# Kernel optimization log

Hardware: AMD Instinct MI355X
Metric: run time of the kernel (lower is better)

Reference implementation:

```python
import jax, jax.numpy as jnp
import numpy as np

NEG_SLOPE = 0.2


def gat_conv(x, src, dst, W, a_src, a_dst, bias, n_nodes):
    # PyG GATConv (heads=1): h = xW; e_ij = LeakyReLU(a_src.h_j + a_dst.h_i)
    # softmax over incoming edges per destination node, then scatter-sum.
    h = x @ W                                  # [N, F]
    alpha_s = h @ a_src                        # [N]
    alpha_d = h @ a_dst                        # [N]
    e = jax.nn.leaky_relu(alpha_s[src] + alpha_d[dst], NEG_SLOPE)  # [E]
    m = jax.ops.segment_max(e, dst, num_segments=n_nodes)
    ex = jnp.exp(e - m[dst])
    denom = jax.ops.segment_sum(ex, dst, num_segments=n_nodes)
    alpha = ex / denom[dst]                    # [E]
    out = jax.ops.segment_sum(alpha[:, None] * h[src], dst, num_segments=n_nodes)
    return out + bias


def setup_inputs() -> dict:
    key = jax.random.key(0)
    ks = jax.random.split(key, 16)
    N, E, F_in = 50000, 800000, 256
    x = jax.random.normal(ks[0], (N, F_in), dtype=jnp.float32)
    edge_index = jax.random.randint(ks[1], (2, E), 0, N, dtype=jnp.int64)

    def glorot(k, shape):
        fan_in, fan_out = shape[0], shape[-1]
        s = jnp.sqrt(6.0 / (fan_in + fan_out))
        return jax.random.uniform(k, shape, jnp.float32, -s, s)

    params = dict(
        W1=glorot(ks[2], (F_in, 128)),
        a1s=glorot(ks[3], (128,)),
        a1d=glorot(ks[4], (128,)),
        b1=jnp.zeros((128,), jnp.float32),
        Wl=glorot(ks[5], (128, 32)),
        bl=jnp.zeros((32,), jnp.float32),
        W2=glorot(ks[6], (32, 16)),
        a2s=glorot(ks[7], (16,)),
        a2d=glorot(ks[8], (16,)),
        b2=jnp.zeros((16,), jnp.float32),
        Wm=glorot(ks[9], (16, 1)),
        bm=jnp.zeros((1,), jnp.float32),
    )
    return {"x": x, "edge_index": edge_index, **params}


def reference(x, edge_index, W1, a1s, a1d, b1, Wl, bl, W2, a2s, a2d, b2, Wm, bm):
    n = x.shape[0]
    loops = jnp.arange(n, dtype=edge_index.dtype)
    src = jnp.concatenate([edge_index[0], loops])  # add_self_loops=True
    dst = jnp.concatenate([edge_index[1], loops])

    h = jax.nn.relu(gat_conv(x, src, dst, W1, a1s, a1d, b1, n))
    h = h @ Wl + bl
    h = jax.nn.relu(gat_conv(h, src, dst, W2, a2s, a2d, b2, n))
    out = h @ Wm + bm                             # MLP([16,1]) = single Linear
    return out.squeeze()
```

## Files before the change

kernel.cpp:

```cpp
#include <hip/hip_runtime.h>
#include <math.h>


#define NEG_SLOPE 0.2f

#define BSHIFT 8
#define BCAP   6144
#define BCAPC  (BCAP + 256)

typedef __attribute__((ext_vector_type(8))) short bf16x8;
typedef __attribute__((ext_vector_type(4))) float f32x4;
typedef __attribute__((ext_vector_type(8))) _Float16 h16x8;

__device__ __forceinline__ unsigned short bf_hi(float f) {
    unsigned u = __float_as_uint(f);
    return (unsigned short)((u + 0x7fffu + ((u >> 16) & 1u)) >> 16);
}
__device__ __forceinline__ float bf_tof(unsigned short s) {
    return __uint_as_float(((unsigned)s) << 16);
}
__device__ __forceinline__ float leaky(float e) {
    return e > 0.f ? e : NEG_SLOPE * e;
}


__launch_bounds__(256)
__global__ void k_bin(const int* __restrict__ src_e, const int* __restrict__ dst_e,
                      int E, int* __restrict__ gcur, unsigned* __restrict__ binned) {
    __shared__ int scnt[256];
    __shared__ int sbase[256];
    int tid = threadIdx.x;
    scnt[tid] = 0;
    __syncthreads();
    int base_e = blockIdx.x * 4096;
    int myd[16];
#pragma unroll
    for (int k = 0; k < 16; ++k) {
        int j = base_e + k * 256 + tid;
        if (j < E) {
            int d = dst_e[j];
            myd[k] = d;
            atomicAdd(&scnt[d >> BSHIFT], 1);
        } else myd[k] = -1;
    }
    __syncthreads();
    int c = scnt[tid];
    sbase[tid] = c ? atomicAdd(&gcur[tid], c) : 0;
    scnt[tid] = 0;
    __syncthreads();
#pragma unroll
    for (int k = 0; k < 16; ++k) {
        int j = base_e + k * 256 + tid;
        if (j >= E) continue;
        int d = myd[k];
        int b = d >> BSHIFT;
        int off = sbase[b] + atomicAdd(&scnt[b], 1);
        if (off < BCAP)
            binned[(size_t)b * BCAP + off] = ((unsigned)src_e[j] << BSHIFT) | (unsigned)(d & 255);
    }
}

__launch_bounds__(256)
__global__ void k_csr(const unsigned* __restrict__ binned, const int* __restrict__ gcur,
                      int N, int* __restrict__ csr, int* __restrict__ rowptr,
                      int* __restrict__ rowend) {
    __shared__ int sdeg[256], s[256], scur[256];
    int b = blockIdx.x, tid = threadIdx.x;
    int node0 = b << BSHIFT;
    int nloc = N - node0; if (nloc > 256) nloc = 256;
    int cnt = gcur[b]; if (cnt > BCAP) cnt = BCAP;
    sdeg[tid] = (tid < nloc) ? 1 : 0;
    __syncthreads();
    const unsigned* bp = binned + (size_t)b * BCAP;
    for (int j = tid; j < cnt; j += 256) atomicAdd(&sdeg[bp[j] & 255], 1);
    __syncthreads();
    int v = sdeg[tid];
    s[tid] = v;
    __syncthreads();
    for (int off = 1; off < 256; off <<= 1) {
        int t = (tid >= off) ? s[tid - off] : 0;
        __syncthreads();
        s[tid] += t;
        __syncthreads();
    }
    int excl = s[tid] - v;
    int rowbase = b * BCAPC;
    if (tid < nloc) {
        rowptr[node0 + tid] = rowbase + excl;
        rowend[node0 + tid] = rowbase + excl + v;
        csr[rowbase + excl] = node0 + tid;
    }
    scur[tid] = excl + 1;
    __syncthreads();
    for (int j = tid; j < cnt; j += 256) {
        unsigned p = bp[j];
        int pos = atomicAdd(&scur[p & 255], 1);
        csr[rowbase + pos] = (int)(p >> BSHIFT);
    }
}


__global__ void k_wcvt(const float* __restrict__ W, short* __restrict__ Wt_hi,
                       short* __restrict__ Wt_lo, int* __restrict__ gcur) {
    if (blockIdx.x == 0) gcur[threadIdx.x] = 0;
    int i = blockIdx.x * 256 + threadIdx.x;
    int k = i >> 7, c = i & 127;
    float v = W[i];
    unsigned short h = bf_hi(v);
    unsigned short l = bf_hi(v - bf_tof(h));
    Wt_hi[c * 256 + k] = (short)h;
    Wt_lo[c * 256 + k] = (short)l;
}


#define LDST 40

__launch_bounds__(256)
__global__ void k_gemm1_mfma(const float* __restrict__ x, const short* __restrict__ Wt_hi,
                             const short* __restrict__ Wt_lo,
                             const float* __restrict__ a1s, const float* __restrict__ a1d,
                             int N, _Float16* __restrict__ h1h,
                             float* __restrict__ as1, float* __restrict__ ad1) {
    __shared__ short Ah[64 * LDST], Al[64 * LDST];
    __shared__ short Bh[128 * LDST], Bl[128 * LDST];
    int tid = threadIdx.x;
    int w = tid >> 6, lane = tid & 63;
    int rowbase = blockIdx.x * 64;

    f32x4 acc[8];
#pragma unroll
    for (int c = 0; c < 8; ++c) acc[c] = (f32x4){0.f, 0.f, 0.f, 0.f};

    int arow = tid >> 2;
    int aq   = tid & 3;
    int agrow = rowbase + arow;
    int fr = lane & 15;
    int fk = lane >> 4;

    for (int ks = 0; ks < 8; ++ks) {
        int k0 = ks * 32;
        __syncthreads();
        {
            float4 u0 = make_float4(0.f, 0.f, 0.f, 0.f), u1 = u0;
            if (agrow < N) {
                const float* p = x + (size_t)agrow * 256 + k0 + aq * 8;
                u0 = *(const float4*)p;
                u1 = *(const float4*)(p + 4);
            }
            float f[8] = {u0.x, u0.y, u0.z, u0.w, u1.x, u1.y, u1.z, u1.w};
            bf16x8 hv, lv;
#pragma unroll
            for (int j = 0; j < 8; ++j) {
                unsigned short h = bf_hi(f[j]);
                unsigned short l = bf_hi(f[j] - bf_tof(h));
                hv[j] = (short)h;
                lv[j] = (short)l;
            }
            *(bf16x8*)&Ah[arow * LDST + aq * 8] = hv;
            *(bf16x8*)&Al[arow * LDST + aq * 8] = lv;
        }
        {
#pragma unroll
            for (int rep = 0; rep < 2; ++rep) {
                int ci = tid + rep * 256;
                int row = ci >> 2, q = ci & 3;
                const short* ph = Wt_hi + row * 256 + k0 + q * 8;
                const short* pl = Wt_lo + row * 256 + k0 + q * 8;
                *(bf16x8*)&Bh[row * LDST + q * 8] = *(const bf16x8*)ph;
                *(bf16x8*)&Bl[row * LDST + q * 8] = *(const bf16x8*)pl;
            }
        }
        __syncthreads();
        bf16x8 a_h = *(const bf16x8*)&Ah[(w * 16 + fr) * LDST + fk * 8];
        bf16x8 a_l = *(const bf16x8*)&Al[(w * 16 + fr) * LDST + fk * 8];
#pragma unroll
        for (int c = 0; c < 8; ++c) {
            bf16x8 b_h = *(const bf16x8*)&Bh[(c * 16 + fr) * LDST + fk * 8];
            bf16x8 b_l = *(const bf16x8*)&Bl[(c * 16 + fr) * LDST + fk * 8];
            acc[c] = __builtin_amdgcn_mfma_f32_16x16x32_bf16(a_h, b_h, acc[c], 0, 0, 0);
            acc[c] = __builtin_amdgcn_mfma_f32_16x16x32_bf16(a_l, b_h, acc[c], 0, 0, 0);
            acc[c] = __builtin_amdgcn_mfma_f32_16x16x32_bf16(a_h, b_l, acc[c], 0, 0, 0);
        }
    }

    float s_[4] = {0.f, 0.f, 0.f, 0.f};
    float d_[4] = {0.f, 0.f, 0.f, 0.f};
#pragma unroll
    for (int c = 0; c < 8; ++c) {
        int col = c * 16 + fr;
        float av = a1s[col], dv = a1d[col];
#pragma unroll
        for (int r = 0; r < 4; ++r) {
            s_[r] += acc[c][r] * av;
            d_[r] += acc[c][r] * dv;
        }
    }
#pragma unroll
    for (int off = 1; off < 16; off <<= 1) {
#pragma unroll
        for (int r = 0; r < 4; ++r) {
            s_[r] += __shfl_xor(s_[r], off);
            d_[r] += __shfl_xor(d_[r], off);
        }
    }
#pragma unroll
    for (int r = 0; r < 4; ++r) {
        int grow = rowbase + w * 16 + fk * 4 + r;
        if (grow < N) {
            _Float16* dst = h1h + (size_t)grow * 128;
#pragma unroll
            for (int c = 0; c < 8; ++c) dst[c * 16 + fr] = (_Float16)acc[c][r];
        }
    }
    if (fr == 0) {
#pragma unroll
        for (int r = 0; r < 4; ++r) {
            int grow = rowbase + w * 16 + fk * 4 + r;
            if (grow < N) { as1[grow] = s_[r]; ad1[grow] = d_[r]; }
        }
    }
}


__global__ void k_agg1(const _Float16* __restrict__ h1h, const float* __restrict__ as1,
                       const float* __restrict__ ad1, const int* __restrict__ rowptr,
                       const int* __restrict__ rowend,
                       const int* __restrict__ csr, const float* __restrict__ b1,
                       int N, float* __restrict__ out1) {
    int wid = (blockIdx.x * blockDim.x + threadIdx.x) >> 6;
    int lane = threadIdx.x & 63;
    if (wid >= N) return;
    int beg = rowptr[wid], end = rowend[wid];
    int cnt = end - beg;
    float adn = ad1[wid];

    int smine = 0;
    float wmine = 0.f;
    if (lane < cnt) {
        smine = csr[beg + lane];
        wmine = __expf(leaky(as1[smine] + adn));
    }
    float den = wmine;
    for (int idx = lane + 64; idx < cnt; idx += 64)
        den += __expf(leaky(as1[csr[beg + idx]] + adn));
#pragma unroll
    for (int off = 32; off; off >>= 1) den += __shfl_xor(den, off);
    float inv = 1.f / den;

    int g = lane >> 4;
    int f8 = lane & 15;
    float acc[8];
#pragma unroll
    for (int k = 0; k < 8; ++k) acc[k] = 0.f;

    int lim = cnt < 64 ? cnt : 64;
    int jb = 0;
    for (; jb + 12 < lim; jb += 16) {
        int j = jb + g;
        int s0 = __shfl(smine, j);
        int s1 = __shfl(smine, j + 4);
        int s2 = __shfl(smine, j + 8);
        int s3 = __shfl(smine, j + 12);
        float w0 = __shfl(wmine, j);
        float w1 = __shfl(wmine, j + 4);
        float w2 = __shfl(wmine, j + 8);
        float w3 = __shfl(wmine, j + 12);
        h16x8 v0 = *(const h16x8*)(h1h + (size_t)s0 * 128 + f8 * 8);
        h16x8 v1 = *(const h16x8*)(h1h + (size_t)s1 * 128 + f8 * 8);
        h16x8 v2 = *(const h16x8*)(h1h + (size_t)s2 * 128 + f8 * 8);
        h16x8 v3 = *(const h16x8*)(h1h + (size_t)s3 * 128 + f8 * 8);
#pragma unroll
        for (int k = 0; k < 8; ++k)
            acc[k] += w0 * (float)v0[k] + w1 * (float)v1[k]
                    + w2 * (float)v2[k] + w3 * (float)v3[k];
    }
    for (; jb < lim; jb += 4) {
        int j = jb + g;
        int s0 = __shfl(smine, j);
        float w0 = __shfl(wmine, j);
        h16x8 v0 = *(const h16x8*)(h1h + (size_t)s0 * 128 + f8 * 8);
#pragma unroll
        for (int k = 0; k < 8; ++k) acc[k] += w0 * (float)v0[k];
    }
    for (int j = 64 + g; j < cnt; j += 4) {
        int s0 = csr[beg + j];
        float w0 = __expf(leaky(as1[s0] + adn));
        h16x8 v0 = *(const h16x8*)(h1h + (size_t)s0 * 128 + f8 * 8);
#pragma unroll
        for (int k = 0; k < 8; ++k) acc[k] += w0 * (float)v0[k];
    }
#pragma unroll
    for (int off = 16; off <= 32; off <<= 1) {
#pragma unroll
        for (int k = 0; k < 8; ++k) acc[k] += __shfl_xor(acc[k], off);
    }
    if (g == 0) {
        const float* bb = b1 + f8 * 8;
        float o[8];
#pragma unroll
        for (int k = 0; k < 8; ++k) o[k] = fmaxf(acc[k] * inv + bb[k], 0.f);
        float* dst = out1 + (size_t)wid * 128 + f8 * 8;
        *(float4*)dst = make_float4(o[0], o[1], o[2], o[3]);
        *(float4*)(dst + 4) = make_float4(o[4], o[5], o[6], o[7]);
    }
}


__launch_bounds__(256)
__global__ void k_mlp(const float* __restrict__ out1, const float* __restrict__ Wl,
                      const float* __restrict__ bl, const float* __restrict__ W2,
                      const float* __restrict__ a2s, const float* __restrict__ a2d,
                      int N, float* __restrict__ h3,
                      float* __restrict__ as2, float* __restrict__ ad2) {
    __shared__ float sWl[128 * 32];
    __shared__ float sW2[32 * 16];
    __shared__ float sbl[32];
    __shared__ float sa2s[16];
    __shared__ float sa2d[16];
    int tid = threadIdx.x;
    for (int i = tid; i < 128 * 32; i += blockDim.x) sWl[i] = Wl[i];
    for (int i = tid; i < 32 * 16; i += blockDim.x) sW2[i] = W2[i];
    if (tid < 32) sbl[tid] = bl[tid];
    if (tid < 16) { sa2s[tid] = a2s[tid]; sa2d[tid] = a2d[tid]; }
    __syncthreads();
    int n = blockIdx.x * blockDim.x + tid;
    if (n >= N) return;

    float h2[32];
#pragma unroll
    for (int j = 0; j < 32; ++j) h2[j] = sbl[j];
    const float4* row = (const float4*)(out1 + (size_t)n * 128);
    for (int k4 = 0; k4 < 32; ++k4) {
        float4 v = row[k4];
        const float* w0 = &sWl[(k4 * 4 + 0) * 32];
        const float* w1 = &sWl[(k4 * 4 + 1) * 32];
        const float* w2 = &sWl[(k4 * 4 + 2) * 32];
        const float* w3 = &sWl[(k4 * 4 + 3) * 32];
#pragma unroll
        for (int j = 0; j < 32; ++j)
            h2[j] += v.x * w0[j] + v.y * w1[j] + v.z * w2[j] + v.w * w3[j];
    }
    float h3l[16];
#pragma unroll
    for (int j = 0; j < 16; ++j) h3l[j] = 0.f;
#pragma unroll
    for (int k = 0; k < 32; ++k) {
        float hv = h2[k];
#pragma unroll
        for (int j = 0; j < 16; ++j) h3l[j] += hv * sW2[k * 16 + j];
    }
    float s = 0.f, d = 0.f;
#pragma unroll
    for (int j = 0; j < 16; ++j) { s += h3l[j] * sa2s[j]; d += h3l[j] * sa2d[j]; }
    float4* h3row = (float4*)(h3 + (size_t)n * 16);
    h3row[0] = make_float4(h3l[0], h3l[1], h3l[2], h3l[3]);
    h3row[1] = make_float4(h3l[4], h3l[5], h3l[6], h3l[7]);
    h3row[2] = make_float4(h3l[8], h3l[9], h3l[10], h3l[11]);
    h3row[3] = make_float4(h3l[12], h3l[13], h3l[14], h3l[15]);
    as2[n] = s;
    ad2[n] = d;
}


__global__ void k_agg2(const float* __restrict__ h3, const float* __restrict__ as2,
                       const float* __restrict__ ad2, const int* __restrict__ rowptr,
                       const int* __restrict__ rowend,
                       const int* __restrict__ csr, const float* __restrict__ b2,
                       const float* __restrict__ Wm, const float* __restrict__ bm,
                       int N, float* __restrict__ out) {
    int wid = (blockIdx.x * blockDim.x + threadIdx.x) >> 6;
    int lane = threadIdx.x & 63;
    if (wid >= N) return;
    int beg = rowptr[wid], end = rowend[wid];
    int cnt = end - beg;
    float adn = ad2[wid];

    int smine = 0;
    float wmine = 0.f;
    if (lane < cnt) {
        smine = csr[beg + lane];
        wmine = __expf(leaky(as2[smine] + adn));
    }
    float den = wmine;
    for (int idx = lane + 64; idx < cnt; idx += 64)
        den += __expf(leaky(as2[csr[beg + idx]] + adn));
#pragma unroll
    for (int off = 32; off; off >>= 1) den += __shfl_xor(den, off);
    float inv = 1.f / den;

    int eg = lane >> 2;
    int f4 = lane & 3;
    float4 acc = make_float4(0.f, 0.f, 0.f, 0.f);
    int lim = cnt < 64 ? cnt : 64;
    int jb = 0;
    for (; jb + 16 < lim; jb += 32) {
        int j = jb + eg;
        int s0 = __shfl(smine, j);
        int s1 = __shfl(smine, j + 16);
        float w0 = __shfl(wmine, j);
        float w1 = __shfl(wmine, j + 16);
        float4 v0 = ((const float4*)(h3 + (size_t)s0 * 16))[f4];
        float4 v1 = ((const float4*)(h3 + (size_t)s1 * 16))[f4];
        acc.x += w0 * v0.x + w1 * v1.x;
        acc.y += w0 * v0.y + w1 * v1.y;
        acc.z += w0 * v0.z + w1 * v1.z;
        acc.w += w0 * v0.w + w1 * v1.w;
    }
    for (; jb < lim; jb += 16) {
        int j = jb + eg;
        int s0 = __shfl(smine, j);
        float w0 = __shfl(wmine, j);
        float4 v0 = ((const float4*)(h3 + (size_t)s0 * 16))[f4];
        acc.x += w0 * v0.x; acc.y += w0 * v0.y;
        acc.z += w0 * v0.z; acc.w += w0 * v0.w;
    }
    for (int j = 64 + eg; j < cnt; j += 16) {
        int s0 = csr[beg + j];
        float w0 = __expf(leaky(as2[s0] + adn));
        float4 v0 = ((const float4*)(h3 + (size_t)s0 * 16))[f4];
        acc.x += w0 * v0.x; acc.y += w0 * v0.y;
        acc.z += w0 * v0.z; acc.w += w0 * v0.w;
    }
#pragma unroll
    for (int off = 4; off <= 32; off <<= 1) {
        acc.x += __shfl_xor(acc.x, off);
        acc.y += __shfl_xor(acc.y, off);
        acc.z += __shfl_xor(acc.z, off);
        acc.w += __shfl_xor(acc.w, off);
    }
    float4 bb = ((const float4*)b2)[f4];
    float4 wm = ((const float4*)Wm)[f4];
    float o0 = fmaxf(acc.x * inv + bb.x, 0.f);
    float o1 = fmaxf(acc.y * inv + bb.y, 0.f);
    float o2 = fmaxf(acc.z * inv + bb.z, 0.f);
    float o3 = fmaxf(acc.w * inv + bb.w, 0.f);
    float v = o0 * wm.x + o1 * wm.y + o2 * wm.z + o3 * wm.w;
    v += __shfl_xor(v, 1);
    v += __shfl_xor(v, 2);
    if (lane == 0) out[wid] = v + bm[0];
}


extern "C" void kernel_launch(void* const* d_in, const int* in_sizes, int n_in,
                              void* d_out, int out_size, void* d_ws, size_t ws_size,
                              hipStream_t stream) {
    const float* x   = (const float*)d_in[0];
    const int*   ei  = (const int*)d_in[1];
    const float* W1  = (const float*)d_in[2];
    const float* a1s = (const float*)d_in[3];
    const float* a1d = (const float*)d_in[4];
    const float* b1  = (const float*)d_in[5];
    const float* Wl  = (const float*)d_in[6];
    const float* bl  = (const float*)d_in[7];
    const float* W2  = (const float*)d_in[8];
    const float* a2s = (const float*)d_in[9];
    const float* a2d = (const float*)d_in[10];
    const float* b2  = (const float*)d_in[11];
    const float* Wm  = (const float*)d_in[12];
    const float* bm  = (const float*)d_in[13];

    int N  = in_sizes[0] / 256;
    int E  = in_sizes[1] / 2;
    int nbuck = (N + 255) >> BSHIFT;
    float* out = (float*)d_out;

    char* w = (char*)d_ws;
    auto alloc = [&](size_t bytes) -> char* {
        char* p = w;
        w += (bytes + 255) & ~(size_t)255;
        return p;
    };
    _Float16* h1h = (_Float16*)alloc((size_t)N * 128 * 2);
    float* out1   = (float*)alloc((size_t)N * 128 * 4);
    float* h3     = (float*)alloc((size_t)N * 16 * 4);
    float* as1    = (float*)alloc((size_t)N * 4);
    float* ad1    = (float*)alloc((size_t)N * 4);
    float* as2    = (float*)alloc((size_t)N * 4);
    float* ad2    = (float*)alloc((size_t)N * 4);
    int*   rowptr = (int*)alloc((size_t)N * 4);
    int*   rowend = (int*)alloc((size_t)N * 4);
    int*   gcur   = (int*)alloc(256 * 4);
    short* Wt_hi  = (short*)alloc((size_t)128 * 256 * 2);
    short* Wt_lo  = (short*)alloc((size_t)128 * 256 * 2);
    unsigned* binned = (unsigned*)alloc((size_t)nbuck * BCAP * 4);
    int*   csr    = (int*)alloc((size_t)nbuck * BCAPC * 4);

    const int* src_e = ei;
    const int* dst_e = ei + E;

    k_wcvt<<<128, 256, 0, stream>>>(W1, Wt_hi, Wt_lo, gcur);
    k_bin<<<(E + 4095) / 4096, 256, 0, stream>>>(src_e, dst_e, E, gcur, binned);
    k_csr<<<nbuck, 256, 0, stream>>>(binned, gcur, N, csr, rowptr, rowend);

    k_gemm1_mfma<<<(N + 63) / 64, 256, 0, stream>>>(x, Wt_hi, Wt_lo, a1s, a1d,
                                                    N, h1h, as1, ad1);
    k_agg1<<<(N + 3) / 4, 256, 0, stream>>>(h1h, as1, ad1, rowptr, rowend, csr, b1, N, out1);
    k_mlp<<<(N + 255) / 256, 256, 0, stream>>>(out1, Wl, bl, W2, a2s, a2d, N, h3, as2, ad2);
    k_agg2<<<(N + 3) / 4, 256, 0, stream>>>(h3, as2, ad2, rowptr, rowend, csr, b2, Wm, bm, N, out);
}
```

Measured before the change: 144.3 us.

## Fuse MLP layer into first aggregation kernel and shrink binning blocks

The linear layer, second GAT projection and attention-score computation are folded into the layer-1 aggregation kernel, so the 128-wide fp32 intermediate no longer goes to global memory and the separate MLP launch is gone. Each wave computes its node's 128->32->16 projection cooperatively using shuffle reductions, with the weights staged in shared memory. Every agg1 block now loads about 18KB of weights into LDS (50000/4 blocks), which adds load traffic and may reduce occupancy. Separately, the binning kernel handles 1024 edges per block instead of 4096, giving more blocks to spread across the GPU.

```diff
diff --git a/kernel.cpp b/kernel.cpp
--- a/kernel.cpp
+++ b/kernel.cpp
@@ -32,10 +32,10 @@
     int tid = threadIdx.x;
     scnt[tid] = 0;
     __syncthreads();
-    int base_e = blockIdx.x * 4096;
-    int myd[16];
-#pragma unroll
-    for (int k = 0; k < 16; ++k) {
+    int base_e = blockIdx.x * 1024;
+    int myd[4];
+#pragma unroll
+    for (int k = 0; k < 4; ++k) {
         int j = base_e + k * 256 + tid;
         if (j < E) {
             int d = dst_e[j];
@@ -49,7 +49,7 @@
     scnt[tid] = 0;
     __syncthreads();
 #pragma unroll
-    for (int k = 0; k < 16; ++k) {
+    for (int k = 0; k < 4; ++k) {
         int j = base_e + k * 256 + tid;
         if (j >= E) continue;
         int d = myd[k];
@@ -222,13 +222,30 @@
 }
 
 
+__launch_bounds__(256)
 __global__ void k_agg1(const _Float16* __restrict__ h1h, const float* __restrict__ as1,
                        const float* __restrict__ ad1, const int* __restrict__ rowptr,
-                       const int* __restrict__ rowend,
-                       const int* __restrict__ csr, const float* __restrict__ b1,
-                       int N, float* __restrict__ out1) {
-    int wid = (blockIdx.x * blockDim.x + threadIdx.x) >> 6;
-    int lane = threadIdx.x & 63;
+                       const int* __restrict__ rowend, const int* __restrict__ csr,
+                       const float* __restrict__ b1, const float* __restrict__ Wl,
+                       const float* __restrict__ bl, const float* __restrict__ W2,
+                       const float* __restrict__ a2s, const float* __restrict__ a2d,
+                       int N, float* __restrict__ h3,
+                       float* __restrict__ as2, float* __restrict__ ad2) {
+    __shared__ float sWl[128 * 32];
+    __shared__ float sW2[32 * 16];
+    __shared__ float sb1[128];
+    __shared__ float sbl[32];
+    __shared__ float sa2s[16], sa2d[16];
+    int tid = threadIdx.x;
+    for (int i = tid; i < 128 * 32; i += 256) sWl[i] = Wl[i];
+    for (int i = tid; i < 32 * 16; i += 256) sW2[i] = W2[i];
+    if (tid < 128) sb1[tid] = b1[tid];
+    if (tid < 32) sbl[tid] = bl[tid];
+    if (tid < 16) { sa2s[tid] = a2s[tid]; sa2d[tid] = a2d[tid]; }
+    __syncthreads();
+
+    int wid = (blockIdx.x * blockDim.x + tid) >> 6;
+    int lane = tid & 63;
     if (wid >= N) return;
     int beg = rowptr[wid], end = rowend[wid];
     int cnt = end - beg;
@@ -294,71 +311,66 @@
 #pragma unroll
         for (int k = 0; k < 8; ++k) acc[k] += __shfl_xor(acc[k], off);
     }
-    if (g == 0) {
-        const float* bb = b1 + f8 * 8;
-        float o[8];
-#pragma unroll
-        for (int k = 0; k < 8; ++k) o[k] = fmaxf(acc[k] * inv + bb[k], 0.f);
-        float* dst = out1 + (size_t)wid * 128 + f8 * 8;
-        *(float4*)dst = make_float4(o[0], o[1], o[2], o[3]);
-        *(float4*)(dst + 4) = make_float4(o[4], o[5], o[6], o[7]);
-    }
-}
-
-
-__launch_bounds__(256)
-__global__ void k_mlp(const float* __restrict__ out1, const float* __restrict__ Wl,
-                      const float* __restrict__ bl, const float* __restrict__ W2,
-                      const float* __restrict__ a2s, const float* __restrict__ a2d,
-                      int N, float* __restrict__ h3,
-                      float* __restrict__ as2, float* __restrict__ ad2) {
-    __shared__ float sWl[128 * 32];
-    __shared__ float sW2[32 * 16];
-    __shared__ float sbl[32];
-    __shared__ float sa2s[16];
-    __shared__ float sa2d[16];
-    int tid = threadIdx.x;
-    for (int i = tid; i < 128 * 32; i += blockDim.x) sWl[i] = Wl[i];
-    for (int i = tid; i < 32 * 16; i += blockDim.x) sW2[i] = W2[i];
-    if (tid < 32) sbl[tid] = bl[tid];
-    if (tid < 16) { sa2s[tid] = a2s[tid]; sa2d[tid] = a2d[tid]; }
-    __syncthreads();
-    int n = blockIdx.x * blockDim.x + tid;
-    if (n >= N) return;
-
-    float h2[32];
-#pragma unroll
-    for (int j = 0; j < 32; ++j) h2[j] = sbl[j];
-    const float4* row = (const float4*)(out1 + (size_t)n * 128);
-    for (int k4 = 0; k4 < 32; ++k4) {
-        float4 v = row[k4];
-        const float* w0 = &sWl[(k4 * 4 + 0) * 32];
-        const float* w1 = &sWl[(k4 * 4 + 1) * 32];
-        const float* w2 = &sWl[(k4 * 4 + 2) * 32];
-        const float* w3 = &sWl[(k4 * 4 + 3) * 32];
-#pragma unroll
-        for (int j = 0; j < 32; ++j)
-            h2[j] += v.x * w0[j] + v.y * w1[j] + v.z * w2[j] + v.w * w3[j];
-    }
+
+    float o[8];
+#pragma unroll
+    for (int k = 0; k < 8; ++k) o[k] = fmaxf(acc[k] * inv + sb1[f8 * 8 + k], 0.f);
+
+    float h2[8];
+#pragma unroll
+    for (int j = 0; j < 8; ++j) h2[j] = 0.f;
+#pragma unroll
+    for (int k = 0; k < 8; ++k) {
+        float ov = o[k];
+        const float* wr = &sWl[(f8 * 8 + k) * 32 + g * 8];
+        float4 wa = *(const float4*)wr;
+        float4 wb = *(const float4*)(wr + 4);
+        h2[0] += ov * wa.x; h2[1] += ov * wa.y; h2[2] += ov * wa.z; h2[3] += ov * wa.w;
+        h2[4] += ov * wb.x; h2[5] += ov * wb.y; h2[6] += ov * wb.z; h2[7] += ov * wb.w;
+    }
+#pragma unroll
+    for (int off = 1; off <= 8; off <<= 1) {
+#pragma unroll
+        for (int j = 0; j < 8; ++j) h2[j] += __shfl_xor(h2[j], off);
+    }
+#pragma unroll
+    for (int j = 0; j < 8; ++j) h2[j] += sbl[g * 8 + j];
+
     float h3l[16];
 #pragma unroll
     for (int j = 0; j < 16; ++j) h3l[j] = 0.f;
 #pragma unroll
-    for (int k = 0; k < 32; ++k) {
+    for (int k = 0; k < 8; ++k) {
         float hv = h2[k];
-#pragma unroll
-        for (int j = 0; j < 16; ++j) h3l[j] += hv * sW2[k * 16 + j];
-    }
+        const float* wr = &sW2[(g * 8 + k) * 16];
+        float4 wa = *(const float4*)wr;
+        float4 wb = *(const float4*)(wr + 4);
+        float4 wc = *(const float4*)(wr + 8);
+        float4 wd = *(const float4*)(wr + 12);
+        h3l[0]  += hv * wa.x; h3l[1]  += hv * wa.y; h3l[2]  += hv * wa.z; h3l[3]  += hv * wa.w;
+        h3l[4]  += hv * wb.x; h3l[5]  += hv * wb.y; h3l[6]  += hv * wb.z; h3l[7]  += hv * wb.w;
+        h3l[8]  += hv * wc.x; h3l[9]  += hv * wc.y; h3l[10] += hv * wc.z; h3l[11] += hv * wc.w;
+        h3l[12] += hv * wd.x; h3l[13] += hv * wd.y; h3l[14] += hv * wd.z; h3l[15] += hv * wd.w;
+    }
+#pragma unroll
+    for (int off = 16; off <= 32; off <<= 1) {
+#pragma unroll
+        for (int j = 0; j < 16; ++j) h3l[j] += __shfl_xor(h3l[j], off);
+    }
+
     float s = 0.f, d = 0.f;
 #pragma unroll
     for (int j = 0; j < 16; ++j) { s += h3l[j] * sa2s[j]; d += h3l[j] * sa2d[j]; }
-    float4* h3row = (float4*)(h3 + (size_t)n * 16);
-    h3row[0] = make_float4(h3l[0], h3l[1], h3l[2], h3l[3]);
-    h3row[1] = make_float4(h3l[4], h3l[5], h3l[6], h3l[7]);
-    h3row[2] = make_float4(h3l[8], h3l[9], h3l[10], h3l[11]);
-    h3row[3] = make_float4(h3l[12], h3l[13], h3l[14], h3l[15]);
-    as2[n] = s;
-    ad2[n] = d;
+
+    if (lane == 0) {
+        float* hp = h3 + (size_t)wid * 16;
+        *(float4*)(hp + 0)  = make_float4(h3l[0], h3l[1], h3l[2], h3l[3]);
+        *(float4*)(hp + 4)  = make_float4(h3l[4], h3l[5], h3l[6], h3l[7]);
+        *(float4*)(hp + 8)  = make_float4(h3l[8], h3l[9], h3l[10], h3l[11]);
+        *(float4*)(hp + 12) = make_float4(h3l[12], h3l[13], h3l[14], h3l[15]);
+        as2[wid] = s;
+        ad2[wid] = d;
+    }
 }
 
 
@@ -471,7 +483,6 @@
         return p;
     };
     _Float16* h1h = (_Float16*)alloc((size_t)N * 128 * 2);
-    float* out1   = (float*)alloc((size_t)N * 128 * 4);
     float* h3     = (float*)alloc((size_t)N * 16 * 4);
     float* as1    = (float*)alloc((size_t)N * 4);
     float* ad1    = (float*)alloc((size_t)N * 4);
@@ -489,12 +500,14 @@
     const int* dst_e = ei + E;
 
     k_wcvt<<<128, 256, 0, stream>>>(W1, Wt_hi, Wt_lo, gcur);
-    k_bin<<<(E + 4095) / 4096, 256, 0, stream>>>(src_e, dst_e, E, gcur, binned);
+    k_bin<<<(E + 1023) / 1024, 256, 0, stream>>>(src_e, dst_e, E, gcur, binned);
     k_csr<<<nbuck, 256, 0, stream>>>(binned, gcur, N, csr, rowptr, rowend);
 
     k_gemm1_mfma<<<(N + 63) / 64, 256, 0, stream>>>(x, Wt_hi, Wt_lo, a1s, a1d,
                                                     N, h1h, as1, ad1);
-    k_agg1<<<(N + 3) / 4, 256, 0, stream>>>(h1h, as1, ad1, rowptr, rowend, csr, b1, N, out1);
-    k_mlp<<<(N + 255) / 256, 256, 0, stream>>>(out1, Wl, bl, W2, a2s, a2d, N, h3, as2, ad2);
-    k_agg2<<<(N + 3) / 4, 256, 0, stream>>>(h3, as2, ad2, rowptr, rowend, csr, b2, Wm, bm, N, out);
-}
+    k_agg1<<<(N + 3) / 4, 256, 0, stream>>>(h1h, as1, ad1, rowptr, rowend, csr,
+                                            b1, Wl, bl, W2, a2s, a2d,
+                                            N, h3, as2, ad2);
+    k_agg2<<<(N + 3) / 4, 256, 0, stream>>>(h3, as2, ad2, rowptr, rowend, csr,
+                                            b2, Wm, bm, N, out);
+}
```

Measured after the change: 216.0 us. +49.7%, slower.

## Merge CSR build and first GEMM into one launch, defer denominator reduction

Applied to the files above, without the earlier changes.

The CSR construction and the first-layer MFMA GEMM are independent, so they now run as one kernel. The first nbuck blocks build the CSR and the remaining blocks do the GEMM, with shared memory overlaid through a union. This removes one launch and its serialization gap, and lets the small CSR grid (196 blocks) overlap with the GEMM blocks. Separately, the softmax denominator's cross-lane shuffle reduction in both aggregation kernels is moved after the feature accumulation, which may let it overlap with the gather latency. The cost is a larger shared-memory footprint for CSR blocks and branch divergence at block level.

```diff
diff --git a/kernel.cpp b/kernel.cpp
--- a/kernel.cpp
+++ b/kernel.cpp
@@ -60,45 +60,6 @@
     }
 }
 
-__launch_bounds__(256)
-__global__ void k_csr(const unsigned* __restrict__ binned, const int* __restrict__ gcur,
-                      int N, int* __restrict__ csr, int* __restrict__ rowptr,
-                      int* __restrict__ rowend) {
-    __shared__ int sdeg[256], s[256], scur[256];
-    int b = blockIdx.x, tid = threadIdx.x;
-    int node0 = b << BSHIFT;
-    int nloc = N - node0; if (nloc > 256) nloc = 256;
-    int cnt = gcur[b]; if (cnt > BCAP) cnt = BCAP;
-    sdeg[tid] = (tid < nloc) ? 1 : 0;
-    __syncthreads();
-    const unsigned* bp = binned + (size_t)b * BCAP;
-    for (int j = tid; j < cnt; j += 256) atomicAdd(&sdeg[bp[j] & 255], 1);
-    __syncthreads();
-    int v = sdeg[tid];
-    s[tid] = v;
-    __syncthreads();
-    for (int off = 1; off < 256; off <<= 1) {
-        int t = (tid >= off) ? s[tid - off] : 0;
-        __syncthreads();
-        s[tid] += t;
-        __syncthreads();
-    }
-    int excl = s[tid] - v;
-    int rowbase = b * BCAPC;
-    if (tid < nloc) {
-        rowptr[node0 + tid] = rowbase + excl;
-        rowend[node0 + tid] = rowbase + excl + v;
-        csr[rowbase + excl] = node0 + tid;
-    }
-    scur[tid] = excl + 1;
-    __syncthreads();
-    for (int j = tid; j < cnt; j += 256) {
-        unsigned p = bp[j];
-        int pos = atomicAdd(&scur[p & 255], 1);
-        csr[rowbase + pos] = (int)(p >> BSHIFT);
-    }
-}
-
 
 __global__ void k_wcvt(const float* __restrict__ W, short* __restrict__ Wt_hi,
                        short* __restrict__ Wt_lo, int* __restrict__ gcur) {
@@ -116,16 +77,58 @@
 #define LDST 40
 
 __launch_bounds__(256)
-__global__ void k_gemm1_mfma(const float* __restrict__ x, const short* __restrict__ Wt_hi,
-                             const short* __restrict__ Wt_lo,
-                             const float* __restrict__ a1s, const float* __restrict__ a1d,
-                             int N, _Float16* __restrict__ h1h,
-                             float* __restrict__ as1, float* __restrict__ ad1) {
-    __shared__ short Ah[64 * LDST], Al[64 * LDST];
-    __shared__ short Bh[128 * LDST], Bl[128 * LDST];
+__global__ void k_csr_gemm(const unsigned* __restrict__ binned, const int* __restrict__ gcur,
+                           int* __restrict__ csr, int* __restrict__ rowptr,
+                           int* __restrict__ rowend, int nbuck,
+                           const float* __restrict__ x, const short* __restrict__ Wt_hi,
+                           const short* __restrict__ Wt_lo,
+                           const float* __restrict__ a1s, const float* __restrict__ a1d,
+                           int N, _Float16* __restrict__ h1h,
+                           float* __restrict__ as1, float* __restrict__ ad1) {
+    __shared__ union {
+        struct { int sdeg[256], s[256], scur[256]; } c;
+        struct { short Ah[64 * LDST], Al[64 * LDST], Bh[128 * LDST], Bl[128 * LDST]; } g;
+    } sm;
     int tid = threadIdx.x;
+
+    if (blockIdx.x < (unsigned)nbuck) {
+        int b = blockIdx.x;
+        int node0 = b << BSHIFT;
+        int nloc = N - node0; if (nloc > 256) nloc = 256;
+        int cnt = gcur[b]; if (cnt > BCAP) cnt = BCAP;
+        sm.c.sdeg[tid] = (tid < nloc) ? 1 : 0;
+        __syncthreads();
+        const unsigned* bp = binned + (size_t)b * BCAP;
+        for (int j = tid; j < cnt; j += 256) atomicAdd(&sm.c.sdeg[bp[j] & 255], 1);
+        __syncthreads();
+        int v = sm.c.sdeg[tid];
+        sm.c.s[tid] = v;
+        __syncthreads();
+        for (int off = 1; off < 256; off <<= 1) {
+            int t = (tid >= off) ? sm.c.s[tid - off] : 0;
+            __syncthreads();
+            sm.c.s[tid] += t;
+            __syncthreads();
+        }
+        int excl = sm.c.s[tid] - v;
+        int rowbase = b * BCAPC;
+        if (tid < nloc) {
+            rowptr[node0 + tid] = rowbase + excl;
+            rowend[node0 + tid] = rowbase + excl + v;
+            csr[rowbase + excl] = node0 + tid;
+        }
+        sm.c.scur[tid] = excl + 1;
+        __syncthreads();
+        for (int j = tid; j < cnt; j += 256) {
+            unsigned p = bp[j];
+            int pos = atomicAdd(&sm.c.scur[p & 255], 1);
+            csr[rowbase + pos] = (int)(p >> BSHIFT);
+        }
+        return;
+    }
+
     int w = tid >> 6, lane = tid & 63;
-    int rowbase = blockIdx.x * 64;
+    int rowbase = (blockIdx.x - nbuck) * 64;
 
     f32x4 acc[8];
 #pragma unroll
@@ -156,8 +159,8 @@
                 hv[j] = (short)h;
                 lv[j] = (short)l;
             }
-            *(bf16x8*)&Ah[arow * LDST + aq * 8] = hv;
-            *(bf16x8*)&Al[arow * LDST + aq * 8] = lv;
+            *(bf16x8*)&sm.g.Ah[arow * LDST + aq * 8] = hv;
+            *(bf16x8*)&sm.g.Al[arow * LDST + aq * 8] = lv;
         }
         {
 #pragma unroll
@@ -166,17 +169,17 @@
                 int row = ci >> 2, q = ci & 3;
                 const short* ph = Wt_hi + row * 256 + k0 + q * 8;
                 const short* pl = Wt_lo + row * 256 + k0 + q * 8;
-                *(bf16x8*)&Bh[row * LDST + q * 8] = *(const bf16x8*)ph;
-                *(bf16x8*)&Bl[row * LDST + q * 8] = *(const bf16x8*)pl;
+                *(bf16x8*)&sm.g.Bh[row * LDST + q * 8] = *(const bf16x8*)ph;
+                *(bf16x8*)&sm.g.Bl[row * LDST + q * 8] = *(const bf16x8*)pl;
             }
         }
         __syncthreads();
-        bf16x8 a_h = *(const bf16x8*)&Ah[(w * 16 + fr) * LDST + fk * 8];
-        bf16x8 a_l = *(const bf16x8*)&Al[(w * 16 + fr) * LDST + fk * 8];
+        bf16x8 a_h = *(const bf16x8*)&sm.g.Ah[(w * 16 + fr) * LDST + fk * 8];
+        bf16x8 a_l = *(const bf16x8*)&sm.g.Al[(w * 16 + fr) * LDST + fk * 8];
 #pragma unroll
         for (int c = 0; c < 8; ++c) {
-            bf16x8 b_h = *(const bf16x8*)&Bh[(c * 16 + fr) * LDST + fk * 8];
-            bf16x8 b_l = *(const bf16x8*)&Bl[(c * 16 + fr) * LDST + fk * 8];
+            bf16x8 b_h = *(const bf16x8*)&sm.g.Bh[(c * 16 + fr) * LDST + fk * 8];
+            bf16x8 b_l = *(const bf16x8*)&sm.g.Bl[(c * 16 + fr) * LDST + fk * 8];
             acc[c] = __builtin_amdgcn_mfma_f32_16x16x32_bf16(a_h, b_h, acc[c], 0, 0, 0);
             acc[c] = __builtin_amdgcn_mfma_f32_16x16x32_bf16(a_l, b_h, acc[c], 0, 0, 0);
             acc[c] = __builtin_amdgcn_mfma_f32_16x16x32_bf16(a_h, b_l, acc[c], 0, 0, 0);
@@ -243,9 +246,6 @@
     float den = wmine;
     for (int idx = lane + 64; idx < cnt; idx += 64)
         den += __expf(leaky(as1[csr[beg + idx]] + adn));
-#pragma unroll
-    for (int off = 32; off; off >>= 1) den += __shfl_xor(den, off);
-    float inv = 1.f / den;
 
     int g = lane >> 4;
     int f8 = lane & 15;
@@ -294,6 +294,10 @@
 #pragma unroll
         for (int k = 0; k < 8; ++k) acc[k] += __shfl_xor(acc[k], off);
     }
+#pragma unroll
+    for (int off = 32; off; off >>= 1) den += __shfl_xor(den, off);
+    float inv = 1.f / den;
+
     if (g == 0) {
         const float* bb = b1 + f8 * 8;
         float o[8];
@@ -384,9 +388,6 @@
     float den = wmine;
     for (int idx = lane + 64; idx < cnt; idx += 64)
         den += __expf(leaky(as2[csr[beg + idx]] + adn));
-#pragma unroll
-    for (int off = 32; off; off >>= 1) den += __shfl_xor(den, off);
-    float inv = 1.f / den;
 
     int eg = lane >> 2;
     int f4 = lane & 3;
@@ -428,6 +429,10 @@
         acc.z += __shfl_xor(acc.z, off);
         acc.w += __shfl_xor(acc.w, off);
     }
+#pragma unroll
+    for (int off = 32; off; off >>= 1) den += __shfl_xor(den, off);
+    float inv = 1.f / den;
+
     float4 bb = ((const float4*)b2)[f4];
     float4 wm = ((const float4*)Wm)[f4];
     float o0 = fmaxf(acc.x * inv + bb.x, 0.f);
@@ -490,10 +495,12 @@
 
     k_wcvt<<<128, 256, 0, stream>>>(W1, Wt_hi, Wt_lo, gcur);
     k_bin<<<(E + 4095) / 4096, 256, 0, stream>>>(src_e, dst_e, E, gcur, binned);
-    k_csr<<<nbuck, 256, 0, stream>>>(binned, gcur, N, csr, rowptr, rowend);
-
-    k_gemm1_mfma<<<(N + 63) / 64, 256, 0, stream>>>(x, Wt_hi, Wt_lo, a1s, a1d,
-                                                    N, h1h, as1, ad1);
+
+    int gemmBlocks = (N + 63) / 64;
+    k_csr_gemm<<<nbuck + gemmBlocks, 256, 0, stream>>>(
+        binned, gcur, csr, rowptr, rowend, nbuck,
+        x, Wt_hi, Wt_lo, a1s, a1d, N, h1h, as1, ad1);
+
     k_agg1<<<(N + 3) / 4, 256, 0, stream>>>(h1h, as1, ad1, rowptr, rowend, csr, b1, N, out1);
     k_mlp<<<(N + 255) / 256, 256, 0, stream>>>(out1, Wl, bl, W2, a2s, a2d, N, h3, as2, ad2);
     k_agg2<<<(N + 3) / 4, 256, 0, stream>>>(h3, as2, ad2, rowptr, rowend, csr, b2, Wm, bm, N, out);
```

Measured after the change: 152.9 us. 1.06x slower.
